# Kernel optimization log

Hardware: AMD Instinct MI355X
Metric: run time of the kernel (lower is better)

The kernel has to match this reference:

```python
import jax, jax.numpy as jnp
import numpy as np
from jax import lax

EPS = 1e-5
HALF = 32
LEVELS = 17  # 16-level quantization of [0,1) -> round(x*255/16) in {0..16}


def setup_inputs() -> dict:
    key = jax.random.key(0)
    ks = jax.random.split(key, 48)
    r = lambda i, s: jax.random.normal(ks[i], s, jnp.float32) * 0.1
    inp = {
        'x': jax.random.uniform(ks[0], (4, 3, 256, 256), jnp.float32),
        # prepare: 1x1 conv (3->32), depthwise 1x1 (per-channel scale), BN, then repeat
        'w1': r(1, (32, 3)), 'b1': r(2, (32,)),
        'w2': 1.0 + r(3, (32,)), 'b2': r(4, (32,)),
        'bn1g': 1.0 + r(5, (32,)), 'bn1b': r(6, (32,)), 'bn1m': r(7, (32,)), 'bn1v': jnp.abs(1.0 + r(8, (32,))),
        'w3': r(9, (32, 32)), 'b3': r(10, (32,)),
        'w4': 1.0 + r(11, (32,)), 'b4': r(12, (32,)),
        'bn2g': 1.0 + r(13, (32,)), 'bn2b': r(14, (32,)), 'bn2m': r(15, (32,)), 'bn2v': jnp.abs(1.0 + r(16, (32,))),
        # downgrade SharedConv: one 3x3 kernel shared across all channels, stride 3, pad 1
        'scw': r(17, (1, 1, 3, 3)), 'scb': r(18, ()),
        # interpolate branch A: SharedConv 5x5 pad 2 + BN
        'iaw': r(19, (1, 1, 5, 5)), 'iabias': r(20, ()),
        'iabg': 1.0 + r(21, (32,)), 'iabb': r(22, (32,)), 'iabm': r(23, (32,)), 'iabv': jnp.abs(1.0 + r(24, (32,))),
        # interpolate branch B
        'ibw': r(25, (1, 1, 5, 5)), 'ibbias': r(26, ()),
        'ibbg': 1.0 + r(27, (32,)), 'ibbb': r(28, (32,)), 'ibbm': r(29, (32,)), 'ibbv': jnp.abs(1.0 + r(30, (32,))),
        'f1g': 1.0 + r(31, (64,)), 'f1b': r(32, (64,)), 'f1m': r(33, (64,)), 'f1v': jnp.abs(1.0 + r(34, (64,))),
        'f2g': 1.0 + r(35, (64,)), 'f2b': r(36, (64,)), 'f2m': r(37, (64,)), 'f2v': jnp.abs(1.0 + r(38, (64,))),
    }
    return inp


def _bn(x, g, b, m, v):
    # eval-mode BatchNorm2d with running stats; params broadcast over [B,C,H,W]
    return (x - m[:, None, None]) * (g[:, None, None] / jnp.sqrt(v[:, None, None] + EPS)) + b[:, None, None]


def _lrelu(x):
    return jnp.where(x >= 0, x, 0.01 * x)


def _mode_pool(x, k=11, stride=1, padding=1):
    # x is already quantized to levels q/16, q in {0..16}; pad with 0 (= level 0)
    x = jnp.pad(x, ((0, 0), (0, 0), (padding, padding), (padding, padding)))
    q = jnp.round(x * 16.0).astype(jnp.int32)  # [B,C,Hp,Wp] integer levels
    onehot = (q[None] == jnp.arange(LEVELS, dtype=jnp.int32)[:, None, None, None, None]).astype(jnp.float32)
    counts = lax.reduce_window(onehot, 0.0, lax.add, (1, 1, 1, k, k), (1, 1, 1, stride, stride), 'VALID')
    # argmax returns the FIRST max -> smallest modal value (torch.mode tie-break)
    return jnp.argmax(counts, axis=0).astype(jnp.float32) / 16.0


def _shared_conv(x, w, b, stride, padding):
    # single kxk kernel shared across all channels (depthwise with tied weight)
    B, C, H, W = x.shape
    y = lax.conv_general_dilated(x.reshape(B * C, 1, H, W), w, (stride, stride),
                                 ((padding, padding), (padding, padding)),
                                 dimension_numbers=('NCHW', 'OIHW', 'NCHW'))
    return y.reshape(B, C, y.shape[2], y.shape[3]) + b


def _ft(x, f1g, f1b, f1m, f1v, f2g, f2b, f2m, f2v):
    x = _bn(x, f1g, f1b, f1m, f1v)
    x = jnp.where(x > 0.1, x, 0.7 * x)  # MaxLeakyReLU(scale=0.7, threshold=0.1)
    x = _bn(x, f2g, f2b, f2m, f2v)
    # EmphaseLocal: gate by local contrast vs 11x11 mean (count_include_pad avg)
    xp = jnp.pad(x, ((0, 0), (0, 0), (5, 5), (5, 5)))
    mean = lax.reduce_window(xp, 0.0, lax.add, (1, 1, 11, 11), (1, 1, 1, 1), 'VALID') / 121.0
    return x * jax.nn.sigmoid(x - mean)


def reference(x, w1, b1, w2, b2, bn1g, bn1b, bn1m, bn1v, w3, b3, w4, b4, bn2g, bn2b, bn2m, bn2v,
              scw, scb, iaw, iabias, iabg, iabb, iabm, iabv, ibw, ibbias, ibbg, ibbb, ibbm, ibbv,
              f1g, f1b, f1m, f1v, f2g, f2b, f2m, f2v):
    B, C, H, W = x.shape
    # prepare: ColorDownsample(16) -> ModePool2d(11,1,1) -> 1x1 conv -> dw 1x1 -> BN -> LReLU (x2)
    d = jnp.round(x * 255.0 / 16.0) * 16.0 / 256.0
    d = _mode_pool(d)
    d = jnp.einsum('bchw,oc->bohw', d, w1) + b1[:, None, None]
    d = d * w2[:, None, None] + b2[:, None, None]
    d = _lrelu(_bn(d, bn1g, bn1b, bn1m, bn1v))
    d = jnp.einsum('bchw,oc->bohw', d, w3) + b3[:, None, None]
    d = d * w4[:, None, None] + b4[:, None, None]
    d = _lrelu(_bn(d, bn2g, bn2b, bn2m, bn2v))

    n = int(np.floor(np.log(min(d.shape[2], d.shape[3])) / np.log(3)))
    score = jnp.zeros((B, 2 * HALF, H, W), jnp.float32)
    for _ in range(n):
        d = _shared_conv(d, scw, scb, 3, 1)  # downgrade
        z = jax.image.resize(d, (B, HALF, H, W), 'bilinear')
        a = _lrelu(_bn(_shared_conv(z, iaw, iabias, 1, 2), iabg, iabb, iabm, iabv))
        bch = _lrelu(_bn(_shared_conv(z, ibw, ibbias, 1, 2), ibbg, ibbb, ibbm, ibbv))
        score = score + jnp.concatenate([a, bch], axis=1)  # Splitter + Stack(1)

    for _ in range(3):
        score = _ft(score, f1g, f1b, f1m, f1v, f2g, f2b, f2m, f2v)
    return score / n
```

## Files before the change

kernel.cpp:

```cpp
#include <hip/hip_runtime.h>
#include <math.h>

#define EPSI 1e-5f

typedef float f32x2 __attribute__((ext_vector_type(2)));

#define P_D1 2048
#define P_D2 (P_D1 + 128*83*83)
#define P_D3 (P_D2 + 128*28*28)
#define P_D4 (P_D3 + 128*10*10)
#define P_D5 (P_D4 + 128*4*4)
#define P_SCORE (P_D5 + 128*2*2)
#define P_D  P_SCORE
#define P_TAB (P_SCORE + 8388608)

__device__ __forceinline__ float rfl(float x) {
  return __builtin_bit_cast(float, __builtin_amdgcn_readfirstlane(__builtin_bit_cast(int, x)));
}

struct PrepArgs { const float* p[39]; };

__global__ __launch_bounds__(256) void k_table(PrepArgs a, float* __restrict__ P,
                                               float* __restrict__ T) {
  __shared__ float Pl[1568];
  int t = threadIdx.x;
  {
    const float *w1=a.p[1],*b1=a.p[2],*w2=a.p[3],*b2=a.p[4],*g1=a.p[5],*bb1=a.p[6],*m1=a.p[7],*v1=a.p[8];
    const float *w3=a.p[9],*b3=a.p[10],*w4=a.p[11],*b4=a.p[12],*g2=a.p[13],*bb2=a.p[14],*m2=a.p[15],*v2=a.p[16];
    for (int i=t;i<96;i+=256){ int o=i/3; float s=g1[o]/sqrtf(v1[o]+EPSI); Pl[i]=w1[i]*w2[o]*s; }
    for (int o=t;o<32;o+=256){ float s=g1[o]/sqrtf(v1[o]+EPSI); Pl[96+o]=(b1[o]*w2[o]+b2[o]-m1[o])*s+bb1[o]; }
    for (int i=t;i<1024;i+=256){ int o2=i/32; float s=g2[o2]/sqrtf(v2[o2]+EPSI); Pl[128+i]=w3[i]*w4[o2]*s; }
    for (int o=t;o<32;o+=256){ float s=g2[o]/sqrtf(v2[o]+EPSI); Pl[1152+o]=(b3[o]*w4[o]+b4[o]-m2[o])*s+bb2[o]; }
    const float *iag=a.p[21],*iab=a.p[22],*iam=a.p[23],*iav=a.p[24],*iabias=a.p[20];
    for (int c=t;c<32;c+=256){ float s=iag[c]/sqrtf(iav[c]+EPSI); Pl[1184+c]=s; Pl[1216+c]=(iabias[0]-iam[c])*s+iab[c]; }
    const float *ibg=a.p[27],*ibb=a.p[28],*ibm=a.p[29],*ibv=a.p[30],*ibbias=a.p[26];
    for (int c=t;c<32;c+=256){ float s=ibg[c]/sqrtf(ibv[c]+EPSI); Pl[1248+c]=s; Pl[1280+c]=(ibbias[0]-ibm[c])*s+ibb[c]; }
    const float *f1g=a.p[31],*f1b=a.p[32],*f1m=a.p[33],*f1v=a.p[34];
    for (int c=t;c<64;c+=256){ float s=f1g[c]/sqrtf(f1v[c]+EPSI); Pl[1312+c]=s; Pl[1376+c]=f1b[c]-f1m[c]*s; }
    const float *f2g=a.p[35],*f2b=a.p[36],*f2m=a.p[37],*f2v=a.p[38];
    for (int c=t;c<64;c+=256){ float s=f2g[c]/sqrtf(f2v[c]+EPSI); Pl[1440+c]=s; Pl[1504+c]=f2b[c]-f2m[c]*s; }
  }
  __syncthreads();
  if (blockIdx.x == 0) {
    for (int i = t; i < 1568; i += 256) P[i] = Pl[i];
  }
  int idx = blockIdx.x*256 + t;
  if (idx >= 4913) return;
  int m0 = idx/289; int rem = idx - m0*289; int m1 = rem/17; int m2 = rem - m1*17;
  float md0 = (float)m0*0.0625f, md1 = (float)m1*0.0625f, md2 = (float)m2*0.0625f;
  const float* A1 = Pl;           const float* C1 = Pl + 96;
  const float* A2 = Pl + 128;     const float* C2 = Pl + 1152;
  float h[32];
  #pragma unroll
  for (int o = 0; o < 32; o++) {
    float v = C1[o] + A1[o*3]*md0 + A1[o*3+1]*md1 + A1[o*3+2]*md2;
    h[o] = (v >= 0.f) ? v : 0.01f*v;
  }
  float* tp = T + (size_t)idx*32;
  #pragma unroll
  for (int o2 = 0; o2 < 32; o2++) {
    float acc = C2[o2];
    #pragma unroll
    for (int o = 0; o < 32; o++) acc += A2[o2*32+o]*h[o];
    tp[o2] = (acc >= 0.f) ? acc : 0.01f*acc;
  }
}

__global__ __launch_bounds__(256) void k_mode_mlp(const float* __restrict__ x,
                                                 const float* __restrict__ T,
                                                 float* __restrict__ dout) {
  __shared__ int qs[3*676];
  __shared__ unsigned CH[3*1326];
  int lx = threadIdx.x, ly = threadIdx.y;
  int tid = ly*16 + lx;
  int tx0 = blockIdx.x*16, ty0 = blockIdx.y*16;
  int b = blockIdx.z;
  for (int k = tid; k < 3*676; k += 256) {
    int cch = k/676; int rem = k - cch*676; int r = rem/26; int cc = rem - r*26;
    int gy = ty0 + r - 1, gx = tx0 + cc - 1;
    int q = 0;
    if ((unsigned)gy < 256u && (unsigned)gx < 256u) {
      float v = x[((size_t)(b*3+cch)*256 + gy)*256 + gx];
      q = (int)rintf(v*255.0f/16.0f);
      q = q < 0 ? 0 : (q > 16 ? 16 : q);
    }
    qs[k] = q;
  }
  __syncthreads();

  if (tid < 156) {
    int half = tid & 1; int rem = tid >> 1;
    int cx = rem % 26; int ch = rem / 26;
    const int* qp = &qs[ch*676 + cx];
    int oy0 = half*8;
    unsigned w0=0, w1=0, w2=0;
    #pragma unroll 1
    for (int r = oy0; r < oy0+11; r++) {
      int q = qp[r*26];
      unsigned inc = 1u << ((q & 7) << 2);
      int sel = q >> 3;
      w0 += (sel==0)?inc:0u; w1 += (sel==1)?inc:0u; w2 += (sel==2)?inc:0u;
    }
    unsigned base = (unsigned)(ch*442 + cx*17 + oy0);
    CH[base] = w0; CH[1326+base] = w1; CH[2652+base] = w2;
    #pragma unroll 1
    for (int i = 1; i < 8; i++) {
      int qr = qp[(oy0+i-1)*26];
      unsigned incr = 1u << ((qr & 7) << 2);
      int selr = qr >> 3;
      w0 -= (selr==0)?incr:0u; w1 -= (selr==1)?incr:0u; w2 -= (selr==2)?incr:0u;
      int qa = qp[(oy0+i+10)*26];
      unsigned inca = 1u << ((qa & 7) << 2);
      int sela = qa >> 3;
      w0 += (sela==0)?inca:0u; w1 += (sela==1)?inca:0u; w2 += (sela==2)?inca:0u;
      CH[base+i] = w0; CH[1326+base+i] = w1; CH[2652+base+i] = w2;
    }
  }
  __syncthreads();

  int oi = ty0 + ly, oj = tx0 + lx;
  if (oi >= 248 || oj >= 248) return;

  int mode[3];
  #pragma unroll
  for (int ch = 0; ch < 3; ch++) {
    unsigned a0=0,a1=0,a2=0,a3=0,a4=0;
    unsigned base = (unsigned)(ch*442 + lx*17 + ly);
    #pragma unroll
    for (int d = 0; d < 11; d++) {
      unsigned r0 = CH[base + d*17];
      unsigned r1 = CH[1326 + base + d*17];
      unsigned r2 = CH[2652 + base + d*17];
      a0 += r0 & 0x0F0F0F0Fu;
      a1 += (r0 >> 4) & 0x0F0F0F0Fu;
      a2 += r1 & 0x0F0F0F0Fu;
      a3 += (r1 >> 4) & 0x0F0F0F0Fu;
      a4 += r2;
    }
    unsigned best = 0u;
    #define KEY(l, wreg) { unsigned cnt = ((wreg) >> ((((l)>>1)&3)*8)) & 255u; \
                           unsigned key = cnt*32u + (31u - (unsigned)(l)); \
                           best = (key > best) ? key : best; }
    KEY(0,a0) KEY(1,a1) KEY(2,a0) KEY(3,a1) KEY(4,a0) KEY(5,a1) KEY(6,a0) KEY(7,a1)
    KEY(8,a2) KEY(9,a3) KEY(10,a2) KEY(11,a3) KEY(12,a2) KEY(13,a3) KEY(14,a2) KEY(15,a3)
    { unsigned cnt = a4 & 255u; unsigned key = cnt*32u + 15u; best = (key > best) ? key : best; }
    #undef KEY
    mode[ch] = 31 - (int)(best & 31u);
  }
  int idx = (mode[0]*17 + mode[1])*17 + mode[2];
  const float* tp = T + (size_t)idx*32;
  size_t ob = ((size_t)(b*32)*248 + oi)*248 + oj;
  #pragma unroll
  for (int o2 = 0; o2 < 32; o2 += 4) {
    float4 v = *(const float4*)(tp + o2);
    dout[ob + (size_t)o2*61504]     = v.x;
    dout[ob + (size_t)(o2+1)*61504] = v.y;
    dout[ob + (size_t)(o2+2)*61504] = v.z;
    dout[ob + (size_t)(o2+3)*61504] = v.w;
  }
}

__global__ void k_down(const float* __restrict__ in, float* __restrict__ out,
                       const float* __restrict__ scw, const float* __restrict__ scb) {
  const int Hin = 248, Hout = 83, total = 128*83*83;
  int idx = blockIdx.x*256 + threadIdx.x;
  if (idx >= total) return;
  float w[9];
  #pragma unroll
  for (int i = 0; i < 9; i++) w[i] = rfl(scw[i]);
  float bias = rfl(scb[0]);
  int j = idx % Hout; int t2 = idx / Hout; int i = t2 % Hout; int p = t2 / Hout;
  const float* base = in + (size_t)p*Hin*Hin;
  float s = bias;
  #pragma unroll
  for (int u = 0; u < 3; u++) {
    int r = 3*i - 1 + u;
    if ((unsigned)r < (unsigned)Hin) {
      #pragma unroll
      for (int v = 0; v < 3; v++) {
        int cc = 3*j - 1 + v;
        if ((unsigned)cc < (unsigned)Hin) s += base[(size_t)r*Hin + cc]*w[u*3+v];
      }
    }
  }
  out[idx] = s;
}

__global__ __launch_bounds__(256) void k_down_rest(const float* __restrict__ in, float* __restrict__ ws,
                                                   const float* __restrict__ scw, const float* __restrict__ scb) {
  __shared__ float buf[6889 + 784 + 100 + 16];
  int tid = threadIdx.x; int p = blockIdx.x;
  float w[9];
  #pragma unroll
  for (int i = 0; i < 9; i++) w[i] = rfl(scw[i]);
  float bias = rfl(scb[0]);
  const float* src = in + (size_t)p*6889;
  for (int k = tid; k < 6889; k += 256) buf[k] = src[k];
  __syncthreads();
  const int HIN[4] = {83,28,10,4}, HOUT[4] = {28,10,4,2};
  const int OIN[4] = {0, 6889, 6889+784, 6889+784+100};
  const size_t GOFF[4] = {P_D2, P_D3, P_D4, P_D5};
  #pragma unroll
  for (int st = 0; st < 4; st++) {
    const int hin = HIN[st], hout = HOUT[st];
    const float* bi = buf + OIN[st];
    float* bo = buf + OIN[st] + hin*hin;
    float* go = ws + GOFF[st] + (size_t)p*(hout*hout);
    for (int k = tid; k < hout*hout; k += 256) {
      int i = k/hout, j = k - i*hout;
      float s = bias;
      #pragma unroll
      for (int u = 0; u < 3; u++) {
        int r = 3*i - 1 + u;
        if ((unsigned)r < (unsigned)hin) {
          #pragma unroll
          for (int v = 0; v < 3; v++) {
            int cc = 3*j - 1 + v;
            if ((unsigned)cc < (unsigned)hin) s += bi[r*hin + cc]*w[u*3+v];
          }
        }
      }
      bo[k] = s; go[k] = s;
    }
    __syncthreads();
  }
}

#define NSP_PACK (83u | (28u<<7) | (10u<<14) | (4u<<21) | (2u<<28))
#define ZROT(r) ((((r)&3) ^ (((r)>>2)&3)) << 3)
__global__ __launch_bounds__(256) void k_accum(const float* __restrict__ ws,
                                               const float* __restrict__ iaw,
                                               const float* __restrict__ ibw,
                                               float* __restrict__ score) {
  __shared__ __align__(16) float hrow[14*96];
  __shared__ __align__(16) float zt[36*96];
  int tid = threadIdx.x;
  int c = blockIdx.y, b = blockIdx.z;
  int tx0 = (blockIdx.x & 3)*64, ty0 = (blockIdx.x >> 2)*32;
  int half = tid >> 7;
  int t2 = tid & 127;
  int lx4 = (t2 & 15)*4, lyt = t2 >> 4;

  const float* wp = half ? ibw : iaw;
  float w[25];
  #pragma unroll
  for (int i = 0; i < 25; i++) w[i] = rfl(wp[i]);
  float s_ = rfl(ws[1184 + half*64 + c]);
  float C_ = rfl(ws[1216 + half*64 + c]);

  int bzy = tid >> 3;
  int bzx0 = tid & 7;

  float acc[16];
  #pragma unroll
  for (int i = 0; i < 16; i++) acc[i] = 0.f;

  size_t off = P_D1;
  #pragma unroll 1
  for (int lvl = 0; lvl < 5; lvl++) {
    const int n = (int)((NSP_PACK >> (7*lvl)) & 127u);
    const float inv = (float)n * (1.f/256.f);
    float f0 = ((float)(ty0-2)+0.5f)*inv - 0.5f;
    float f1 = ((float)(ty0+33)+0.5f)*inv - 0.5f;
    int yb0 = min(max((int)floorf(f0),0), n-2);
    int yb1 = min(max((int)floorf(f1),0), n-2);
    int rows = yb1 - yb0 + 2;
    const float* dp = ws + off + (size_t)(b*32+c)*(n*n);

    #pragma unroll 1
    for (int k = tid; k < rows*68; k += 256) {
      int r = k/68, zx = k - r*68;
      int gx = tx0 + zx - 2;
      float h = 0.f;
      if ((unsigned)gx < 256u) {
        float f = ((float)gx + 0.5f)*inv - 0.5f;
        float ff = floorf(f);
        int i0 = (int)ff;
        int xb = min(max(i0,0), n-2);
        float wx = (i0 < 0) ? 0.f : (i0 > n-2 ? 1.f : f - ff);
        const float* rp = dp + (yb0 + r)*n + xb;
        h = rp[0] + wx*(rp[1] - rp[0]);
      }
      hrow[r*96 + ((r&3)<<3) + zx] = h;
    }
    __syncthreads();

    {
      int gy = ty0 - 2 + bzy;
      float f = ((float)gy + 0.5f)*inv - 0.5f;
      float ff = floorf(f);
      int i0 = (int)ff;
      int yb = min(max(i0,0), n-2);
      float wy = (i0 < 0) ? 0.f : (i0 > n-2 ? 1.f : f - ff);
      bool vy = ((unsigned)gy < 256u);
      int rel = yb - yb0;
      int ra = rel*96 + ((rel&3)<<3);
      int rb = (rel+1)*96 + (((rel+1)&3)<<3);
      int zr0 = bzy*96 + ZROT(bzy);
      #pragma unroll
      for (int s = 0; s < 9; s++) {
        int zx = bzx0 + s*8;
        if (zx < 68) {
          float v = 0.f;
          if (vy) { float a = hrow[ra + zx], bb = hrow[rb + zx]; v = a + wy*(bb - a); }
          zt[zr0 + zx] = v;
        }
      }
      #pragma unroll 1
      for (int k = tid; k < 4*68; k += 256) {
        int zy = 32 + k/68; int zx = k - (k/68)*68;
        int gy2 = ty0 - 2 + zy;
        float v = 0.f;
        if ((unsigned)gy2 < 256u) {
          float f2 = ((float)gy2 + 0.5f)*inv - 0.5f;
          float ff2 = floorf(f2);
          int i02 = (int)ff2;
          int yb2 = min(max(i02,0), n-2);
          float wy2 = (i02 < 0) ? 0.f : (i02 > n-2 ? 1.f : f2 - ff2);
          int rel2 = yb2 - yb0;
          float a = hrow[rel2*96 + ((rel2&3)<<3) + zx];
          float bb = hrow[(rel2+1)*96 + (((rel2+1)&3)<<3) + zx];
          v = a + wy2*(bb - a);
        }
        zt[zy*96 + ZROT(zy) + zx] = v;
      }
    }
    __syncthreads();

    f32x2 cc2[4][2];
    #pragma unroll
    for (int p = 0; p < 4; p++)
      #pragma unroll
      for (int j2 = 0; j2 < 2; j2++) cc2[p][j2] = (f32x2)(0.f);
    #pragma unroll
    for (int zr = 0; zr < 8; zr++) {
      int row = 4*lyt + zr;
      int o = row*96 + ZROT(row) + lx4;
      float4 a0 = *(const float4*)&zt[o];
      float4 a1 = *(const float4*)&zt[o+4];
      float zz[8] = {a0.x,a0.y,a0.z,a0.w,a1.x,a1.y,a1.z,a1.w};
      #pragma unroll
      for (int p = 0; p < 4; p++) {
        int r = zr - p;
        if (r >= 0 && r < 5) {
          #pragma unroll
          for (int v = 0; v < 5; v++) {
            float wv = w[r*5+v];
            cc2[p][0] += (f32x2){zz[v],   zz[v+1]} * wv;
            cc2[p][1] += (f32x2){zz[v+2], zz[v+3]} * wv;
          }
        }
      }
    }
    #pragma unroll
    for (int p = 0; p < 4; p++)
      #pragma unroll
      for (int j2 = 0; j2 < 2; j2++) {
        f32x2 v2 = cc2[p][j2]*s_ + C_;
        #pragma unroll
        for (int e = 0; e < 2; e++) {
          float v = v2[e];
          acc[p*4 + j2*2 + e] += (v >= 0.f) ? v : 0.01f*v;
        }
      }
    off += (size_t)128*n*n;
  }
  int oy = ty0 + 4*lyt, ox = tx0 + lx4;
  size_t base = ((size_t)(b*64 + half*32 + c)*256 + oy)*256 + ox;
  #pragma unroll
  for (int p = 0; p < 4; p++)
    *(float4*)&score[base + (size_t)p*256] = make_float4(acc[p*4],acc[p*4+1],acc[p*4+2],acc[p*4+3]);
}

__global__ __launch_bounds__(256) void k_ft(const float* __restrict__ in,
                                            float* __restrict__ out,
                                            const float* __restrict__ P, float scale) {
  __shared__ float Bf[16*271];
  int tid = threadIdx.x;
  int c = blockIdx.y, b = blockIdx.z;
  int ty0 = blockIdx.x * 16;
  float fs1 = rfl(P[1312+c]), fc1 = rfl(P[1376+c]), fs2 = rfl(P[1440+c]), fc2 = rfl(P[1504+c]);
  const float* ip = in + (size_t)(b*64 + c)*65536 + tid;

  if (tid < 160) {
    int r = tid / 10, q = tid - r*10;
    Bf[r*271 + (q < 5 ? q : 256 + q)] = 0.f;
  }

  float yreg[16];
  float win[11];
  float run = 0.f;
  #pragma unroll
  for (int s = 0; s < 26; s++) {
    int gy = ty0 + s - 5;
    float yv = 0.f;
    if ((unsigned)gy < 256u) {
      float t = ip[(size_t)gy*256]*fs1 + fc1;
      t = (t > 0.1f) ? t : 0.7f*t;
      yv = t*fs2 + fc2;
    }
    win[s % 11] = yv;
    run += yv;
    if (s >= 5 && s <= 20) yreg[s-5] = yv;
    if (s >= 10) {
      Bf[(s-10)*271 + 5 + tid] = run;
      run -= win[(s-10) % 11];
    }
  }
  __syncthreads();

  const size_t ob = (size_t)(b*64 + c)*65536 + (size_t)ty0*256 + tid;
  #pragma unroll
  for (int r = 0; r < 16; r++) {
    const float* bfr = Bf + r*271 + tid;
    float s = bfr[0];
    #pragma unroll
    for (int d = 1; d < 11; d++) s += bfr[d];
    float y = yreg[r];
    float sig = 1.f/(1.f + __expf(-(y - s*(1.f/121.f))));
    out[ob + (size_t)r*256] = y*sig*scale;
  }
}

extern "C" void kernel_launch(void* const* d_in, const int* in_sizes, int n_in,
                              void* d_out, int out_size, void* d_ws, size_t ws_size,
                              hipStream_t stream) {
  const float* x = (const float*)d_in[0];
  float* ws = (float*)d_ws;
  float* out = (float*)d_out;

  PrepArgs pa;
  for (int i = 0; i < 39; i++) pa.p[i] = (const float*)d_in[i];
  k_table<<<dim3(20), dim3(256), 0, stream>>>(pa, ws, ws + P_TAB);

  k_mode_mlp<<<dim3(16,16,4), dim3(16,16), 0, stream>>>(x, ws + P_TAB, ws + P_D);

  const float* scw = (const float*)d_in[17];
  const float* scb = (const float*)d_in[18];
  {
    int total = 128*83*83;
    k_down<<<dim3((total+255)/256), dim3(256), 0, stream>>>(ws + P_D, ws + P_D1, scw, scb);
  }
  k_down_rest<<<dim3(128), dim3(256), 0, stream>>>(ws + P_D1, ws, scw, scb);

  k_accum<<<dim3(32,32,4), dim3(256), 0, stream>>>(ws, (const float*)d_in[19],
                                                   (const float*)d_in[25], ws + P_SCORE);

  k_ft<<<dim3(16,64,4), dim3(256), 0, stream>>>(ws + P_SCORE, out, ws, 1.f);
  k_ft<<<dim3(16,64,4), dim3(256), 0, stream>>>(out, ws + P_SCORE, ws, 1.f);
  k_ft<<<dim3(16,64,4), dim3(256), 0, stream>>>(ws + P_SCORE, out, ws, 0.2f);
}
```

Before: 361.2 us.

## Fuse three ft passes into one streaming row-pipelined kernel

Replaces the three k_ft launches with one k_ft3 kernel. It streams rows through three chained ft stages, passing each stage's output to the next in registers and double-buffered shared-memory row sums. This removes two full 64-channel 256x256 intermediate writes and reads to global memory, plus two launches. In exchange, each 32-row tile recomputes a 15-row halo and takes a __syncthreads every row, which serialises work within the block.

```diff
diff --git a/kernel.cpp b/kernel.cpp
--- a/kernel.cpp
+++ b/kernel.cpp
@@ -372,53 +372,92 @@
     *(float4*)&score[base + (size_t)p*256] = make_float4(acc[p*4],acc[p*4+1],acc[p*4+2],acc[p*4+3]);
 }
 
-__global__ __launch_bounds__(256) void k_ft(const float* __restrict__ in,
-                                            float* __restrict__ out,
-                                            const float* __restrict__ P, float scale) {
-  __shared__ float Bf[16*271];
+__global__ __launch_bounds__(256) void k_ft3(const float* __restrict__ in,
+                                             float* __restrict__ out,
+                                             const float* __restrict__ P) {
+  __shared__ float L1[2][272], L2[2][272], L3[2][272];
   int tid = threadIdx.x;
   int c = blockIdx.y, b = blockIdx.z;
-  int ty0 = blockIdx.x * 16;
+  int ty0 = blockIdx.x * 32;
   float fs1 = rfl(P[1312+c]), fc1 = rfl(P[1376+c]), fs2 = rfl(P[1440+c]), fc2 = rfl(P[1504+c]);
   const float* ip = in + (size_t)(b*64 + c)*65536 + tid;
-
-  if (tid < 160) {
-    int r = tid / 10, q = tid - r*10;
-    Bf[r*271 + (q < 5 ? q : 256 + q)] = 0.f;
-  }
-
-  float yreg[16];
-  float win[11];
-  float run = 0.f;
-  #pragma unroll
-  for (int s = 0; s < 26; s++) {
-    int gy = ty0 + s - 5;
-    float yv = 0.f;
-    if ((unsigned)gy < 256u) {
-      float t = ip[(size_t)gy*256]*fs1 + fc1;
-      t = (t > 0.1f) ? t : 0.7f*t;
-      yv = t*fs2 + fc2;
-    }
-    win[s % 11] = yv;
-    run += yv;
-    if (s >= 5 && s <= 20) yreg[s-5] = yv;
-    if (s >= 10) {
-      Bf[(s-10)*271 + 5 + tid] = run;
-      run -= win[(s-10) % 11];
-    }
-  }
-  __syncthreads();
-
-  const size_t ob = (size_t)(b*64 + c)*65536 + (size_t)ty0*256 + tid;
-  #pragma unroll
-  for (int r = 0; r < 16; r++) {
-    const float* bfr = Bf + r*271 + tid;
-    float s = bfr[0];
-    #pragma unroll
-    for (int d = 1; d < 11; d++) s += bfr[d];
-    float y = yreg[r];
-    float sig = 1.f/(1.f + __expf(-(y - s*(1.f/121.f))));
-    out[ob + (size_t)r*256] = y*sig*scale;
+  float* op = out + (size_t)(b*64 + c)*65536 + tid;
+
+  if (tid < 60) {
+    int bufi = tid/20, rem = tid - bufi*20;
+    int sl = rem/10, q = rem - sl*10;
+    int idx = (q < 5 ? q : 256 + q);
+    float* Lp = (bufi == 0) ? &L1[sl][0] : ((bufi == 1) ? &L2[sl][0] : &L3[sl][0]);
+    Lp[idx] = 0.f;
+  }
+
+  float r1[11], r2[11], r3[11];
+  float run1 = 0.f, run2 = 0.f, run3 = 0.f, pend2 = 0.f, pend3 = 0.f;
+  const float inv121 = 1.f/121.f;
+
+  #pragma unroll
+  for (int s = 0; s < 64; s++) {
+    if (s <= 61) {
+      int gy = ty0 - 15 + s;
+      float yv = 0.f;
+      if ((unsigned)gy < 256u) {
+        float t = ip[(size_t)gy*256]*fs1 + fc1;
+        t = (t > 0.1f) ? t : 0.7f*t;
+        yv = t*fs2 + fc2;
+      }
+      r1[s % 11] = yv;
+      run1 += yv;
+      if (s >= 10) { L1[s&1][5+tid] = run1; run1 -= r1[(s-10) % 11]; }
+    }
+    if (s >= 21 && s <= 62) L2[s&1][5+tid] = pend2;
+    if (s >= 32)            L3[s&1][5+tid] = pend3;
+    __syncthreads();
+    if (s >= 10 && s <= 61) {
+      const float* lp = &L1[s&1][tid];
+      float hs = lp[0];
+      #pragma unroll
+      for (int d = 1; d < 11; d++) hs += lp[d];
+      float yc = r1[(s-5) % 11];
+      float o1 = yc * (1.f/(1.f + __expf(-(yc - hs*inv121))));
+      int c1 = ty0 - 20 + s;
+      float y2 = 0.f;
+      if ((unsigned)c1 < 256u) {
+        float t = o1*fs1 + fc1;
+        t = (t > 0.1f) ? t : 0.7f*t;
+        y2 = t*fs2 + fc2;
+      }
+      r2[(s-10) % 11] = y2;
+      run2 += y2;
+      if (s >= 20) { pend2 = run2; run2 -= r2[(s-20) % 11]; }
+    }
+    if (s >= 21 && s <= 62) {
+      const float* lp = &L2[s&1][tid];
+      float hs = lp[0];
+      #pragma unroll
+      for (int d = 1; d < 11; d++) hs += lp[d];
+      float yc = r2[(s-16) % 11];
+      float o2 = yc * (1.f/(1.f + __expf(-(yc - hs*inv121))));
+      int c2 = ty0 - 26 + s;
+      float y3 = 0.f;
+      if ((unsigned)c2 < 256u) {
+        float t = o2*fs1 + fc1;
+        t = (t > 0.1f) ? t : 0.7f*t;
+        y3 = t*fs2 + fc2;
+      }
+      r3[(s-21) % 11] = y3;
+      run3 += y3;
+      if (s >= 31) { pend3 = run3; run3 -= r3[(s-31) % 11]; }
+    }
+    if (s >= 32) {
+      const float* lp = &L3[s&1][tid];
+      float hs = lp[0];
+      #pragma unroll
+      for (int d = 1; d < 11; d++) hs += lp[d];
+      float yc = r3[(s-27) % 11];
+      float o3 = yc * (1.f/(1.f + __expf(-(yc - hs*inv121))));
+      int c3 = ty0 - 32 + s;
+      op[(size_t)c3*256] = o3 * 0.2f;
+    }
   }
 }
 
@@ -446,7 +485,5 @@
   k_accum<<<dim3(32,32,4), dim3(256), 0, stream>>>(ws, (const float*)d_in[19],
                                                    (const float*)d_in[25], ws + P_SCORE);
 
-  k_ft<<<dim3(16,64,4), dim3(256), 0, stream>>>(ws + P_SCORE, out, ws, 1.f);
-  k_ft<<<dim3(16,64,4), dim3(256), 0, stream>>>(out, ws + P_SCORE, ws, 1.f);
-  k_ft<<<dim3(16,64,4), dim3(256), 0, stream>>>(ws + P_SCORE, out, ws, 0.2f);
-}
+  k_ft3<<<dim3(8,64,4), dim3(256), 0, stream>>>(ws + P_SCORE, out, ws);
+}
```

After: 381.7 us. 5.7% more time.
